# Performance work log

Hardware: AMD Instinct MI355X
Metric: run time of the kernel (lower is better)

Reference implementation:

```python
import jax, jax.numpy as jnp
import numpy as np


def setup_inputs() -> dict:
    key = jax.random.key(0)
    ks = jax.random.split(key, 6)
    B, Q, K = 4, 512, 1024
    Dq, Dk, Dv, H = 512, 512, 512, 128
    return {
        "queries": jax.random.normal(ks[0], (B, Q, Dq), dtype=jnp.float32),
        "keys": jax.random.normal(ks[1], (B, K, Dk), dtype=jnp.float32),
        "values": jax.random.normal(ks[2], (B, K, Dv), dtype=jnp.float32),
        "W_q": jax.random.normal(ks[3], (Dq, H), dtype=jnp.float32) / np.sqrt(Dq),
        "W_k": jax.random.normal(ks[4], (Dk, H), dtype=jnp.float32) / np.sqrt(Dk),
        "w_v": jax.random.normal(ks[5], (H,), dtype=jnp.float32) / np.sqrt(H),
    }


def reference(queries, keys, values, W_q, W_k, w_v):
    # Additive (Bahdanau) attention.
    q = jnp.einsum("bqd,dh->bqh", queries, W_q)          # [B,Q,H]
    k = jnp.einsum("bkd,dh->bkh", keys, W_k)             # [B,K,H]
    features = jnp.tanh(q[:, :, None, :] + k[:, None, :, :])  # [B,Q,K,H]
    scores = jnp.einsum("bqkh,h->bqk", features, w_v)    # [B,Q,K]
    attn = jax.nn.softmax(scores, axis=-1)               # [B,Q,K]
    return jnp.einsum("bqk,bkv->bqv", attn, values)      # [B,Q,Dv]
```

## Files before the change

kernel.cpp:

```cpp
#include <hip/hip_runtime.h>

#define BB   4
#define QS   512
#define KSZ  1024
#define DD   512
#define HH   128
#define DVV  512
#define KPN  16

typedef unsigned int uint;
typedef unsigned short ushort;
typedef unsigned long long ull;
typedef __attribute__((ext_vector_type(8)))  short short8;
typedef __attribute__((ext_vector_type(16))) float f32x16;

__device__ __forceinline__ float rcp_fast(float x)  { return __builtin_amdgcn_rcpf(x); }
__device__ __forceinline__ float exp2_fast(float x) { return __builtin_amdgcn_exp2f(x); }

__device__ __forceinline__ void split1(float v, ushort& h, ushort& l) {
    uint u = __float_as_uint(v);
    h = (ushort)(u >> 16);
    float r = v - __uint_as_float(u & 0xffff0000u);
    l = (ushort)(__float_as_uint(r) >> 16);
}

#define NSQ  (BB * QS * DD / 4 / 256)
#define NSK  (BB * KSZ * DD / 4 / 256)
#define NWT  128
#define NPJ  192
#define NVT  (BB * (KSZ / 32) * (DVV / 32))

__global__ __launch_bounds__(256) void split_kernel(
    const float* __restrict__ q, const float* __restrict__ k,
    const float* __restrict__ Wq, const float* __restrict__ Wk,
    ushort* __restrict__ qh, ushort* __restrict__ ql,
    ushort* __restrict__ kh, ushort* __restrict__ kl,
    ushort* __restrict__ wqh, ushort* __restrict__ wql,
    ushort* __restrict__ wkh, ushort* __restrict__ wkl)
{
    const int id  = blockIdx.x;
    const int tid = threadIdx.x;

    if (id < NSQ + NSK) {
        const float* src; ushort* dh; ushort* dl; size_t i;
        if (id < NSQ) { src = q; dh = qh; dl = ql; i = (size_t)id * 256 + tid; }
        else          { src = k; dh = kh; dl = kl; i = (size_t)(id - NSQ) * 256 + tid; }
        float4 v = ((const float4*)src)[i];
        ushort h0,h1,h2,h3,l0,l1,l2,l3;
        split1(v.x,h0,l0); split1(v.y,h1,l1); split1(v.z,h2,l2); split1(v.w,h3,l3);
        *(ushort4*)&dh[i * 4] = make_ushort4(h0,h1,h2,h3);
        *(ushort4*)&dl[i * 4] = make_ushort4(l0,l1,l2,l3);
        return;
    }
    __shared__ float Ts[32][33];
    int t = id - (NSQ + NSK);
    const float* W; ushort* dh; ushort* dl;
    if (t < 64) { W = Wq; dh = wqh; dl = wql; }
    else        { W = Wk; dh = wkh; dl = wkl; t -= 64; }
    const int d0 = (t >> 2) * 32, h0 = (t & 3) * 32;
    {
        const int dd = tid >> 3, c4 = (tid & 7) * 4;
        float4 v = *(const float4*)&W[(size_t)(d0 + dd) * HH + h0 + c4];
        Ts[dd][c4 + 0] = v.x; Ts[dd][c4 + 1] = v.y;
        Ts[dd][c4 + 2] = v.z; Ts[dd][c4 + 3] = v.w;
    }
    __syncthreads();
    {
        const int hh = tid >> 3, d4 = (tid & 7) * 4;
        ushort h[4], l[4];
        #pragma unroll
        for (int i = 0; i < 4; i++) split1(Ts[d4 + i][hh], h[i], l[i]);
        size_t o = (size_t)(h0 + hh) * DD + d0 + d4;
        *(ushort4*)&dh[o] = make_ushort4(h[0], h[1], h[2], h[3]);
        *(ushort4*)&dl[o] = make_ushort4(l[0], l[1], l[2], l[3]);
    }
}

__global__ __launch_bounds__(256) void projvt_kernel(
    const ushort* __restrict__ qh, const ushort* __restrict__ ql,
    const ushort* __restrict__ kh, const ushort* __restrict__ kl,
    const ushort* __restrict__ wqh, const ushort* __restrict__ wql,
    const ushort* __restrict__ wkh, const ushort* __restrict__ wkl,
    const float* __restrict__ val,
    float* __restrict__ eq, float* __restrict__ ek,
    ushort* __restrict__ vhi, ushort* __restrict__ vlo)
{
    const int id  = blockIdx.x;
    const int tid = threadIdx.x;

    if (id >= NPJ) {
        __shared__ float Ts[32][33];
        const int t   = id - NPJ;
        const int b   = t >> 9;
        const int rem = t & 511;
        const int k0  = (rem >> 4) * 32;
        const int n0  = (rem & 15) * 32;
        {
            const int kk = tid >> 3, n4 = (tid & 7) * 4;
            float4 v = *(const float4*)&val[((size_t)b * KSZ + k0 + kk) * DVV + n0 + n4];
            Ts[kk][n4 + 0] = v.x; Ts[kk][n4 + 1] = v.y;
            Ts[kk][n4 + 2] = v.z; Ts[kk][n4 + 3] = v.w;
        }
        __syncthreads();
        {
            const int nn = tid >> 3, k4 = (tid & 7) * 4;
            ushort h[4], l[4];
            #pragma unroll
            for (int i = 0; i < 4; i++) split1(Ts[k4 + i][nn], h[i], l[i]);
            size_t o = ((size_t)b * DVV + n0 + nn) * KSZ + k0 + k4;
            *(ushort4*)&vhi[o] = make_ushort4(h[0], h[1], h[2], h[3]);
            *(ushort4*)&vlo[o] = make_ushort4(l[0], l[1], l[2], l[3]);
        }
        return;
    }

    const int w = tid >> 6, lane = tid & 63;
    const int row = lane & 31, kg = lane >> 5;
    const int gw = id * 4 + w;

    const ushort *pa_h, *pa_l, *pb_h, *pb_l; float* op; int m0, nt;
    if (gw < 256) {
        m0 = (gw >> 2) * 32; nt = gw & 3;
        pa_h = qh; pa_l = ql; pb_h = wqh; pb_l = wql; op = eq;
    } else {
        const int g = gw - 256;
        m0 = (g >> 2) * 32; nt = g & 3;
        pa_h = kh; pa_l = kl; pb_h = wkh; pb_l = wkl; op = ek;
    }

    const ushort* ah_p = pa_h + (size_t)(m0 + row) * DD + kg * 8;
    const ushort* al_p = pa_l + (size_t)(m0 + row) * DD + kg * 8;
    const ushort* bh_p = pb_h + (size_t)(nt * 32 + row) * DD + kg * 8;
    const ushort* bl_p = pb_l + (size_t)(nt * 32 + row) * DD + kg * 8;

    f32x16 acc;
    #pragma unroll
    for (int i = 0; i < 16; i++) acc[i] = 0.f;

    #pragma unroll 8
    for (int ks = 0; ks < DD; ks += 16) {
        short8 ah = *(const short8*)(ah_p + ks);
        short8 al = *(const short8*)(al_p + ks);
        short8 bh = *(const short8*)(bh_p + ks);
        short8 bl = *(const short8*)(bl_p + ks);
        acc = __builtin_amdgcn_mfma_f32_32x32x16_bf16(ah, bh, acc, 0, 0, 0);
        acc = __builtin_amdgcn_mfma_f32_32x32x16_bf16(ah, bl, acc, 0, 0, 0);
        acc = __builtin_amdgcn_mfma_f32_32x32x16_bf16(al, bh, acc, 0, 0, 0);
    }

    const float C2L = 2.8853900817779268f;
    float* ob = op + (size_t)m0 * HH + nt * 32;
    #pragma unroll
    for (int r = 0; r < 16; r++) {
        const int rb = (r & 3) + 8 * (r >> 2) + 4 * kg;
        ob[(size_t)rb * HH + row] = exp2_fast(acc[r] * C2L);
    }
}

__global__ __launch_bounds__(256, 4) void spv_kernel(
    const float* __restrict__ eq, const float* __restrict__ ek,
    const float* __restrict__ wv,
    const ushort* __restrict__ vhi, const ushort* __restrict__ vlo,
    float* __restrict__ opart, float* __restrict__ rsp)
{
    __shared__ float  eqs[32][132];
    __shared__ float  eks[32][132];
    __shared__ ushort PhS[32][36];
    __shared__ ushort PlS[32][36];

    const int id  = blockIdx.x;
    const int kp  = id & 15;
    const int b   = (id >> 4) & 3;
    const int qt  = id >> 6;

    const int tid  = threadIdx.x;
    const int w    = tid >> 6, lane = tid & 63;
    const int tq   = tid >> 4;
    const int tk   = tid & 15;
    const int wn   = w * 128;
    const int arow = lane & 31;
    const int akg  = lane >> 5;

    const float* eqg = eq + ((size_t)b * QS + qt * 32) * HH;
    #pragma unroll
    for (int i = 0; i < 4; i++) {
        int f = tid + i * 256;
        *(float4*)&eqs[f >> 5][(f & 31) * 4] =
            *(const float4*)&eqg[(size_t)(f >> 5) * HH + (f & 31) * 4];
    }
    const float* ekg = ek + ((size_t)b * KSZ + kp * 64) * HH;
    #pragma unroll
    for (int i = 0; i < 4; i++) {
        int f = tid + i * 256;
        *(float4*)&eks[f >> 5][(f & 31) * 4] =
            *(const float4*)&ekg[(size_t)(f >> 5) * HH + (f & 31) * 4];
    }
    __syncthreads();

    f32x16 acc[4];
    #pragma unroll
    for (int n = 0; n < 4; n++) {
        #pragma unroll
        for (int i = 0; i < 16; i++) acc[n][i] = 0.f;
    }
    float rowacc0 = 0.f, rowacc1 = 0.f;

    const size_t vrow0 = ((size_t)b * DVV + wn + arow) * KSZ + kp * 64 + akg * 8;
    const ushort* vhb = vhi + vrow0;
    const ushort* vlb = vlo + vrow0;

#define SGROUP(eqv, ekv, sacc) { \
    float u0 = fminf(fmaf((eqv).x, (ekv).x, 1.0f), 3e7f); \
    float u1 = fminf(fmaf((eqv).y, (ekv).y, 1.0f), 3e7f); \
    float u2 = fminf(fmaf((eqv).z, (ekv).z, 1.0f), 3e7f); \
    float u3 = fminf(fmaf((eqv).w, (ekv).w, 1.0f), 3e7f); \
    float p01 = u0 * u1, p23 = u2 * u3; \
    float n01 = fmaf(wv4.x, u1, wv4.y * u0); \
    float n23 = fmaf(wv4.z, u3, wv4.w * u2); \
    float Nn = fmaf(n01, p23, n23 * p01); \
    sacc = fmaf(Nn, rcp_fast(p01 * p23), sacc); }

    #pragma unroll
    for (int s = 0; s < 2; s++) {
        float s00 = 0.f, s01 = 0.f, s10 = 0.f, s11 = 0.f;
        #pragma unroll 4
        for (int h = 0; h < HH; h += 4) {
            float4 wv4 = *(const float4*)&wv[h];
            float4 eqa = *(const float4*)&eqs[tq][h];
            float4 eqb = *(const float4*)&eqs[tq + 16][h];
            float4 eka = *(const float4*)&eks[tk][h];
            float4 ekb = *(const float4*)&eks[tk + 16][h];
            SGROUP(eqa, eka, s00);
            SGROUP(eqa, ekb, s01);
            SGROUP(eqb, eka, s10);
            SGROUP(eqb, ekb, s11);
        }
        {
            const float CN = -2.8853900817779268f;
            float p00 = exp2_fast(s00 * CN);
            float p01v = exp2_fast(s01 * CN);
            float p10 = exp2_fast(s10 * CN);
            float p11 = exp2_fast(s11 * CN);
            ushort hh, ll;
            split1(p00,  hh, ll); PhS[tq][tk]           = hh; PlS[tq][tk]           = ll;
            split1(p01v, hh, ll); PhS[tq][tk + 16]      = hh; PlS[tq][tk + 16]      = ll;
            split1(p10,  hh, ll); PhS[tq + 16][tk]      = hh; PlS[tq + 16][tk]      = ll;
            split1(p11,  hh, ll); PhS[tq + 16][tk + 16] = hh; PlS[tq + 16][tk + 16] = ll;
            rowacc0 += p00 + p01v;
            rowacc1 += p10 + p11;
        }
        __syncthreads();

        if (s == 0) {
            #pragma unroll
            for (int i = 0; i < 4; i++) {
                int f = tid + i * 256;
                *(float4*)&eks[f >> 5][(f & 31) * 4] =
                    *(const float4*)&ekg[(size_t)(32 + (f >> 5)) * HH + (f & 31) * 4];
            }
        }

        short8 ah0, al0, ah1, al1;
        { const ull* p = (const ull*)&PhS[arow][akg * 8];
          ((ull*)&ah0)[0] = p[0]; ((ull*)&ah0)[1] = p[1]; }
        { const ull* p = (const ull*)&PlS[arow][akg * 8];
          ((ull*)&al0)[0] = p[0]; ((ull*)&al0)[1] = p[1]; }
        { const ull* p = (const ull*)&PhS[arow][16 + akg * 8];
          ((ull*)&ah1)[0] = p[0]; ((ull*)&ah1)[1] = p[1]; }
        { const ull* p = (const ull*)&PlS[arow][16 + akg * 8];
          ((ull*)&al1)[0] = p[0]; ((ull*)&al1)[1] = p[1]; }
        #pragma unroll
        for (int nb = 0; nb < 4; nb++) {
            const size_t o = (size_t)nb * 32 * KSZ + (size_t)s * 32;
            short8 vh0 = *(const short8*)(vhb + o);
            short8 vl0 = *(const short8*)(vlb + o);
            short8 vh1 = *(const short8*)(vhb + o + 16);
            short8 vl1 = *(const short8*)(vlb + o + 16);
            acc[nb] = __builtin_amdgcn_mfma_f32_32x32x16_bf16(ah0, vh0, acc[nb], 0, 0, 0);
            acc[nb] = __builtin_amdgcn_mfma_f32_32x32x16_bf16(ah0, vl0, acc[nb], 0, 0, 0);
            acc[nb] = __builtin_amdgcn_mfma_f32_32x32x16_bf16(al0, vh0, acc[nb], 0, 0, 0);
            acc[nb] = __builtin_amdgcn_mfma_f32_32x32x16_bf16(ah1, vh1, acc[nb], 0, 0, 0);
            acc[nb] = __builtin_amdgcn_mfma_f32_32x32x16_bf16(ah1, vl1, acc[nb], 0, 0, 0);
            acc[nb] = __builtin_amdgcn_mfma_f32_32x32x16_bf16(al1, vh1, acc[nb], 0, 0, 0);
        }
        __syncthreads();
    }
#undef SGROUP

    #pragma unroll
    for (int m = 8; m; m >>= 1) {
        rowacc0 += __shfl_xor(rowacc0, m);
        rowacc1 += __shfl_xor(rowacc1, m);
    }
    if (tk == 0) {
        rsp[((size_t)b * QS + qt * 32 + tq) * KPN + kp]      = rowacc0;
        rsp[((size_t)b * QS + qt * 32 + tq + 16) * KPN + kp] = rowacc1;
    }

    float* ob = opart + (((size_t)kp * BB + b) * QS + qt * 32) * DVV + wn;
    #pragma unroll
    for (int nb = 0; nb < 4; nb++) {
        #pragma unroll
        for (int r = 0; r < 16; r++) {
            const int rb = (r & 3) + 8 * (r >> 2) + 4 * akg;
            ob[(size_t)rb * DVV + nb * 32 + arow] = acc[nb][r];
        }
    }
}

__global__ __launch_bounds__(256) void norm_kernel(
    const float* __restrict__ opart, const float* __restrict__ rsp,
    float* __restrict__ outp)
{
    const int i  = blockIdx.x * 256 + threadIdx.x;
    const int n4 = (i & 127) * 4;
    const int q  = (i >> 7) & (QS - 1);
    const int b  = i >> 16;

    const float* rp = rsp + ((size_t)b * QS + q) * KPN;
    float s = 0.f;
    #pragma unroll
    for (int j = 0; j < KPN / 4; j++) {
        float4 r = *(const float4*)(rp + j * 4);
        s += r.x + r.y + r.z + r.w;
    }
    float inv = rcp_fast(s);

    float ox = 0.f, oy = 0.f, oz = 0.f, ow = 0.f;
    #pragma unroll
    for (int kp = 0; kp < KPN; kp++) {
        float4 v = *(const float4*)&opart[(((size_t)kp * BB + b) * QS + q) * DVV + n4];
        ox += v.x; oy += v.y; oz += v.z; ow += v.w;
    }
    float4 res = make_float4(ox * inv, oy * inv, oz * inv, ow * inv);
    *(float4*)&outp[((size_t)b * QS + q) * DVV + n4] = res;
}

extern "C" void kernel_launch(void* const* d_in, const int* in_sizes, int n_in,
                              void* d_out, int out_size, void* d_ws, size_t ws_size,
                              hipStream_t stream)
{
    const float* queries = (const float*)d_in[0];
    const float* keys    = (const float*)d_in[1];
    const float* values  = (const float*)d_in[2];
    const float* Wq      = (const float*)d_in[3];
    const float* Wk      = (const float*)d_in[4];
    const float* wv      = (const float*)d_in[5];
    float* out = (float*)d_out;

    float*  eq    = (float*)d_ws;
    float*  ek    = eq  + (size_t)BB * QS * HH;
    float*  rsp   = ek  + (size_t)BB * KSZ * HH;
    float*  opart = rsp + (size_t)BB * QS * KPN;
    ushort* vhi = (ushort*)(opart + (size_t)KPN * BB * QS * DVV);
    ushort* vlo = vhi + (size_t)BB * KSZ * DVV;
    ushort* qh  = vlo + (size_t)BB * KSZ * DVV;
    ushort* ql  = qh  + (size_t)BB * QS * DD;
    ushort* kh  = ql  + (size_t)BB * QS * DD;
    ushort* kl  = kh  + (size_t)BB * KSZ * DD;
    ushort* wqh = kl  + (size_t)BB * KSZ * DD;
    ushort* wql = wqh + (size_t)HH * DD;
    ushort* wkh = wql + (size_t)HH * DD;
    ushort* wkl = wkh + (size_t)HH * DD;

    split_kernel<<<dim3(NSQ + NSK + NWT), 256, 0, stream>>>(
        queries, keys, Wq, Wk, qh, ql, kh, kl, wqh, wql, wkh, wkl);

    projvt_kernel<<<dim3(NPJ + NVT), 256, 0, stream>>>(
        qh, ql, kh, kl, wqh, wql, wkh, wkl, values, eq, ek, vhi, vlo);

    spv_kernel<<<dim3(1024), 256, 0, stream>>>(eq, ek, wv, vhi, vlo, opart, rsp);

    norm_kernel<<<dim3(1024), 256, 0, stream>>>(opart, rsp, out);
}
```

Measured before the change: 153.6 us.

## Pipeline score compute with MFMA and pack score math into float2 ops

Restructures the score/PV loop in spv_kernel so that computing the second key sub-tile's scores is interleaved with the MFMA accumulation of the first sub-tile, with register double-buffering of V loads and a register prefetch of the next key tile. The score math is rewritten in paired float2 form (with a permuted w_v layout produced in split_kernel and a matching permuted store of exp(2k)) so the compiler can emit packed FMA/mul instructions. The per-element 3e7 clamp moves to a 5e4 clamp at projection time. This aims to overlap VALU transcendental work with matrix-core work and cut VALU instruction count, at the cost of more registers and a changed numerical clamp.

```diff
diff --git a/kernel.cpp b/kernel.cpp
--- a/kernel.cpp
+++ b/kernel.cpp
@@ -13,9 +13,12 @@
 typedef unsigned long long ull;
 typedef __attribute__((ext_vector_type(8)))  short short8;
 typedef __attribute__((ext_vector_type(16))) float f32x16;
+typedef __attribute__((ext_vector_type(2)))  float f32x2;
 
 __device__ __forceinline__ float rcp_fast(float x)  { return __builtin_amdgcn_rcpf(x); }
 __device__ __forceinline__ float exp2_fast(float x) { return __builtin_amdgcn_exp2f(x); }
+__device__ __forceinline__ f32x2 lo2(float4 v) { return (f32x2){v.x, v.y}; }
+__device__ __forceinline__ f32x2 hi2(float4 v) { return (f32x2){v.z, v.w}; }
 
 __device__ __forceinline__ void split1(float v, ushort& h, ushort& l) {
     uint u = __float_as_uint(v);
@@ -24,6 +27,10 @@
     l = (ushort)(__float_as_uint(r) >> 16);
 }
 
+__device__ __forceinline__ int hperm(int h) {
+    return (h & ~3) | ((h & 1) << 1) | ((h >> 1) & 1);
+}
+
 #define NSQ  (BB * QS * DD / 4 / 256)
 #define NSK  (BB * KSZ * DD / 4 / 256)
 #define NWT  128
@@ -33,6 +40,7 @@
 __global__ __launch_bounds__(256) void split_kernel(
     const float* __restrict__ q, const float* __restrict__ k,
     const float* __restrict__ Wq, const float* __restrict__ Wk,
+    const float* __restrict__ wv, float* __restrict__ wvp,
     ushort* __restrict__ qh, ushort* __restrict__ ql,
     ushort* __restrict__ kh, ushort* __restrict__ kl,
     ushort* __restrict__ wqh, ushort* __restrict__ wql,
@@ -54,6 +62,7 @@
     }
     __shared__ float Ts[32][33];
     int t = id - (NSQ + NSK);
+    if (t == 0 && tid < HH) wvp[hperm(tid)] = wv[tid];
     const float* W; ushort* dh; ushort* dl;
     if (t < 64) { W = Wq; dh = wqh; dl = wql; }
     else        { W = Wk; dh = wkh; dl = wkl; t -= 64; }
@@ -150,16 +159,17 @@
 
     const float C2L = 2.8853900817779268f;
     float* ob = op + (size_t)m0 * HH + nt * 32;
+    const int prow = hperm(row);
     #pragma unroll
     for (int r = 0; r < 16; r++) {
         const int rb = (r & 3) + 8 * (r >> 2) + 4 * kg;
-        ob[(size_t)rb * HH + row] = exp2_fast(acc[r] * C2L);
+        ob[(size_t)rb * HH + prow] = fminf(exp2_fast(acc[r] * C2L), 5.0e4f);
     }
 }
 
 __global__ __launch_bounds__(256, 4) void spv_kernel(
     const float* __restrict__ eq, const float* __restrict__ ek,
-    const float* __restrict__ wv,
+    const float* __restrict__ wvp,
     const ushort* __restrict__ vhi, const ushort* __restrict__ vlo,
     float* __restrict__ opart, float* __restrict__ rsp)
 {
@@ -195,6 +205,13 @@
         *(float4*)&eks[f >> 5][(f & 31) * 4] =
             *(const float4*)&ekg[(size_t)(f >> 5) * HH + (f & 31) * 4];
     }
+
+    float4 eknxt[4];
+    #pragma unroll
+    for (int i = 0; i < 4; i++) {
+        int f = tid + i * 256;
+        eknxt[i] = *(const float4*)&ekg[(size_t)(32 + (f >> 5)) * HH + (f & 31) * 4];
+    }
     __syncthreads();
 
     f32x16 acc[4];
@@ -209,83 +226,99 @@
     const ushort* vhb = vhi + vrow0;
     const ushort* vlb = vlo + vrow0;
 
-#define SGROUP(eqv, ekv, sacc) { \
-    float u0 = fminf(fmaf((eqv).x, (ekv).x, 1.0f), 3e7f); \
-    float u1 = fminf(fmaf((eqv).y, (ekv).y, 1.0f), 3e7f); \
-    float u2 = fminf(fmaf((eqv).z, (ekv).z, 1.0f), 3e7f); \
-    float u3 = fminf(fmaf((eqv).w, (ekv).w, 1.0f), 3e7f); \
-    float p01 = u0 * u1, p23 = u2 * u3; \
-    float n01 = fmaf(wv4.x, u1, wv4.y * u0); \
-    float n23 = fmaf(wv4.z, u3, wv4.w * u2); \
-    float Nn = fmaf(n01, p23, n23 * p01); \
-    sacc = fmaf(Nn, rcp_fast(p01 * p23), sacc); }
-
-    #pragma unroll
-    for (int s = 0; s < 2; s++) {
-        float s00 = 0.f, s01 = 0.f, s10 = 0.f, s11 = 0.f;
-        #pragma unroll 4
-        for (int h = 0; h < HH; h += 4) {
-            float4 wv4 = *(const float4*)&wv[h];
-            float4 eqa = *(const float4*)&eqs[tq][h];
-            float4 eqb = *(const float4*)&eqs[tq + 16][h];
-            float4 eka = *(const float4*)&eks[tk][h];
-            float4 ekb = *(const float4*)&eks[tk + 16][h];
-            SGROUP(eqa, eka, s00);
-            SGROUP(eqa, ekb, s01);
-            SGROUP(eqb, eka, s10);
-            SGROUP(eqb, ekb, s11);
+    const f32x2 one2 = {1.0f, 1.0f};
+
+#define SGROUP(eq4, ek4, sacc) { \
+    f32x2 u02 = __builtin_elementwise_fma(lo2(eq4), lo2(ek4), one2); \
+    f32x2 u13 = __builtin_elementwise_fma(hi2(eq4), hi2(ek4), one2); \
+    f32x2 p_  = u02 * u13; \
+    f32x2 n_  = __builtin_elementwise_fma(wA, u13, wB * u02); \
+    float N_  = fmaf(n_.x, p_.y, n_.y * p_.x); \
+    sacc = fmaf(N_, rcp_fast(p_.x * p_.y), sacc); }
+
+#define HITER(h) { \
+    float4 wp4 = *(const float4*)&wvp[h]; \
+    f32x2 wA = lo2(wp4), wB = hi2(wp4); \
+    float4 eqa = *(const float4*)&eqs[tq][h]; \
+    float4 eqb = *(const float4*)&eqs[tq + 16][h]; \
+    float4 eka = *(const float4*)&eks[tk][h]; \
+    float4 ekb = *(const float4*)&eks[tk + 16][h]; \
+    SGROUP(eqa, eka, s00); SGROUP(eqa, ekb, s01); \
+    SGROUP(eqb, eka, s10); SGROUP(eqb, ekb, s11); }
+
+#define VLOAD(vh_, vl_, g, sp) { \
+    const size_t o_ = (size_t)((g) >> 1) * 32 * KSZ + (size_t)(sp) * 32 + ((g) & 1) * 16; \
+    vh_ = *(const short8*)(vhb + o_); \
+    vl_ = *(const short8*)(vlb + o_); }
+
+#define MFMASUB(g, vh_, vl_) { \
+    const int k2_ = (g) & 1, nb_ = (g) >> 1; \
+    short8 ah_, al_; \
+    { const ull* p = (const ull*)&PhS[arow][k2_ * 16 + akg * 8]; \
+      ((ull*)&ah_)[0] = p[0]; ((ull*)&ah_)[1] = p[1]; } \
+    { const ull* p = (const ull*)&PlS[arow][k2_ * 16 + akg * 8]; \
+      ((ull*)&al_)[0] = p[0]; ((ull*)&al_)[1] = p[1]; } \
+    acc[nb_] = __builtin_amdgcn_mfma_f32_32x32x16_bf16(ah_, vh_, acc[nb_], 0, 0, 0); \
+    acc[nb_] = __builtin_amdgcn_mfma_f32_32x32x16_bf16(ah_, vl_, acc[nb_], 0, 0, 0); \
+    acc[nb_] = __builtin_amdgcn_mfma_f32_32x32x16_bf16(al_, vh_, acc[nb_], 0, 0, 0); }
+
+#define PWRITE() { \
+    const float CN = -2.8853900817779268f; \
+    float p00 = exp2_fast(s00 * CN), p01v = exp2_fast(s01 * CN); \
+    float p10 = exp2_fast(s10 * CN), p11  = exp2_fast(s11 * CN); \
+    ushort hh_, ll_; \
+    split1(p00,  hh_, ll_); PhS[tq][tk]           = hh_; PlS[tq][tk]           = ll_; \
+    split1(p01v, hh_, ll_); PhS[tq][tk + 16]      = hh_; PlS[tq][tk + 16]      = ll_; \
+    split1(p10,  hh_, ll_); PhS[tq + 16][tk]      = hh_; PlS[tq + 16][tk]      = ll_; \
+    split1(p11,  hh_, ll_); PhS[tq + 16][tk + 16] = hh_; PlS[tq + 16][tk + 16] = ll_; \
+    rowacc0 += p00 + p01v; rowacc1 += p10 + p11; }
+
+    float s00, s01, s10, s11;
+
+    s00 = s01 = s10 = s11 = 0.f;
+    #pragma unroll 4
+    for (int h = 0; h < HH; h += 4) HITER(h);
+    __syncthreads();
+    PWRITE();
+    #pragma unroll
+    for (int i = 0; i < 4; i++) {
+        int f = tid + i * 256;
+        *(float4*)&eks[f >> 5][(f & 31) * 4] = eknxt[i];
+    }
+    __syncthreads();
+
+    s00 = s01 = s10 = s11 = 0.f;
+    {
+        short8 vh, vl, vhn, vln;
+        VLOAD(vh, vl, 0, 0);
+        #pragma unroll
+        for (int g = 0; g < 8; ++g) {
+            #pragma unroll
+            for (int hh = 0; hh < 4; ++hh) HITER(g * 16 + hh * 4);
+            if (g < 7) { VLOAD(vhn, vln, g + 1, 0); }
+            MFMASUB(g, vh, vl);
+            if (g < 7) { vh = vhn; vl = vln; }
         }
-        {
-            const float CN = -2.8853900817779268f;
-            float p00 = exp2_fast(s00 * CN);
-            float p01v = exp2_fast(s01 * CN);
-            float p10 = exp2_fast(s10 * CN);
-            float p11 = exp2_fast(s11 * CN);
-            ushort hh, ll;
-            split1(p00,  hh, ll); PhS[tq][tk]           = hh; PlS[tq][tk]           = ll;
-            split1(p01v, hh, ll); PhS[tq][tk + 16]      = hh; PlS[tq][tk + 16]      = ll;
-            split1(p10,  hh, ll); PhS[tq + 16][tk]      = hh; PlS[tq + 16][tk]      = ll;
-            split1(p11,  hh, ll); PhS[tq + 16][tk + 16] = hh; PlS[tq + 16][tk + 16] = ll;
-            rowacc0 += p00 + p01v;
-            rowacc1 += p10 + p11;
+    }
+    __syncthreads();
+    PWRITE();
+    __syncthreads();
+
+    {
+        short8 vh, vl, vhn, vln;
+        VLOAD(vh, vl, 0, 1);
+        #pragma unroll
+        for (int g = 0; g < 8; ++g) {
+            if (g < 7) { VLOAD(vhn, vln, g + 1, 1); }
+            MFMASUB(g, vh, vl);
+            if (g < 7) { vh = vhn; vl = vln; }
         }
-        __syncthreads();
-
-        if (s == 0) {
-            #pragma unroll
-            for (int i = 0; i < 4; i++) {
-                int f = tid + i * 256;
-                *(float4*)&eks[f >> 5][(f & 31) * 4] =
-                    *(const float4*)&ekg[(size_t)(32 + (f >> 5)) * HH + (f & 31) * 4];
-            }
-        }
-
-        short8 ah0, al0, ah1, al1;
-        { const ull* p = (const ull*)&PhS[arow][akg * 8];
-          ((ull*)&ah0)[0] = p[0]; ((ull*)&ah0)[1] = p[1]; }
-        { const ull* p = (const ull*)&PlS[arow][akg * 8];
-          ((ull*)&al0)[0] = p[0]; ((ull*)&al0)[1] = p[1]; }
-        { const ull* p = (const ull*)&PhS[arow][16 + akg * 8];
-          ((ull*)&ah1)[0] = p[0]; ((ull*)&ah1)[1] = p[1]; }
-        { const ull* p = (const ull*)&PlS[arow][16 + akg * 8];
-          ((ull*)&al1)[0] = p[0]; ((ull*)&al1)[1] = p[1]; }
-        #pragma unroll
-        for (int nb = 0; nb < 4; nb++) {
-            const size_t o = (size_t)nb * 32 * KSZ + (size_t)s * 32;
-            short8 vh0 = *(const short8*)(vhb + o);
-            short8 vl0 = *(const short8*)(vlb + o);
-            short8 vh1 = *(const short8*)(vhb + o + 16);
-            short8 vl1 = *(const short8*)(vlb + o + 16);
-            acc[nb] = __builtin_amdgcn_mfma_f32_32x32x16_bf16(ah0, vh0, acc[nb], 0, 0, 0);
-            acc[nb] = __builtin_amdgcn_mfma_f32_32x32x16_bf16(ah0, vl0, acc[nb], 0, 0, 0);
-            acc[nb] = __builtin_amdgcn_mfma_f32_32x32x16_bf16(al0, vh0, acc[nb], 0, 0, 0);
-            acc[nb] = __builtin_amdgcn_mfma_f32_32x32x16_bf16(ah1, vh1, acc[nb], 0, 0, 0);
-            acc[nb] = __builtin_amdgcn_mfma_f32_32x32x16_bf16(ah1, vl1, acc[nb], 0, 0, 0);
-            acc[nb] = __builtin_amdgcn_mfma_f32_32x32x16_bf16(al1, vh1, acc[nb], 0, 0, 0);
-        }
-        __syncthreads();
     }
 #undef SGROUP
+#undef HITER
+#undef VLOAD
+#undef MFMASUB
+#undef PWRITE
 
     #pragma unroll
     for (int m = 8; m; m >>= 1) {
@@ -351,7 +384,8 @@
     float*  eq    = (float*)d_ws;
     float*  ek    = eq  + (size_t)BB * QS * HH;
     float*  rsp   = ek  + (size_t)BB * KSZ * HH;
-    float*  opart = rsp + (size_t)BB * QS * KPN;
+    float*  wvp   = rsp + (size_t)BB * QS * KPN;
+    float*  opart = wvp + 256;
     ushort* vhi = (ushort*)(opart + (size_t)KPN * BB * QS * DVV);
     ushort* vlo = vhi + (size_t)BB * KSZ * DVV;
     ushort* qh  = vlo + (size_t)BB * KSZ * DVV;
@@ -364,12 +398,12 @@
     ushort* wkl = wkh + (size_t)HH * DD;
 
     split_kernel<<<dim3(NSQ + NSK + NWT), 256, 0, stream>>>(
-        queries, keys, Wq, Wk, qh, ql, kh, kl, wqh, wql, wkh, wkl);
+        queries, keys, Wq, Wk, wv, wvp, qh, ql, kh, kl, wqh, wql, wkh, wkl);
 
     projvt_kernel<<<dim3(NPJ + NVT), 256, 0, stream>>>(
         qh, ql, kh, kl, wqh, wql, wkh, wkl, values, eq, ek, vhi, vlo);
 
-    spv_kernel<<<dim3(1024), 256, 0, stream>>>(eq, ek, wv, vhi, vlo, opart, rsp);
+    spv_kernel<<<dim3(1024), 256, 0, stream>>>(eq, ek, wvp, vhi, vlo, opart, rsp);
 
     norm_kernel<<<dim3(1024), 256, 0, stream>>>(opart, rsp, out);
 }
```

Measured after the change: 157.8 us. 2.8% more time.
